# Kernel tuning notes

Hardware: AMD Instinct MI355X
Metric: run time of the kernel (lower is better)

The kernel has to match this reference:

```python
import jax, jax.numpy as jnp
import numpy as np

B, T, H = 4, 2048, 1024
NH, NKV, HD = 16, 4, 64  # heads, kv heads, head_dim

def setup_inputs() -> dict:
    key = jax.random.key(0)
    ks = jax.random.split(key, 5)
    s = 0.02
    return {
        "x": jax.random.normal(ks[0], (B, T, H), dtype=jnp.float32),
        "wq": jax.random.normal(ks[1], (H, NH * HD), dtype=jnp.float32) * s,
        "wk": jax.random.normal(ks[2], (H, NKV * HD), dtype=jnp.float32) * s,
        "wv": jax.random.normal(ks[3], (H, NKV * HD), dtype=jnp.float32) * s,
        "wo": jax.random.normal(ks[4], (NH * HD, H), dtype=jnp.float32) * s,
    }

def reference(x, wq, wk, wv, wo):
    b, t, _ = x.shape
    q = (x @ wq).reshape(b, t, NH, HD).transpose(0, 2, 1, 3)    # [B,NH,T,HD]
    k = (x @ wk).reshape(b, t, NKV, HD).transpose(0, 2, 1, 3)   # [B,NKV,T,HD]
    v = (x @ wv).reshape(b, t, NKV, HD).transpose(0, 2, 1, 3)
    n_rep = NH // NKV
    # repeat_kv: expand each kv head n_rep times along the head axis
    k_rep = jnp.repeat(k, n_rep, axis=1)                        # [B,NH,T,HD]
    v_rep = jnp.repeat(v, n_rep, axis=1)
    scale = 1.0 / np.sqrt(HD).astype(np.float32)
    scores = jnp.einsum('bhqd,bhkd->bhqk', q, k_rep) * scale    # [B,NH,T,T]
    key_pos = jnp.arange(t)[None, :]
    q_pos = jnp.arange(t)[:, None]  # past_len = 0 (no kv cache)
    causal = key_pos > q_pos                                    # [T,T]
    scores = jnp.where(causal[None, None], -jnp.inf, scores)
    probs = jax.nn.softmax(scores, axis=-1)                     # dropout is identity (eval / rate 0)
    attn = jnp.einsum('bhqk,bhkd->bhqd', probs, v_rep)          # [B,NH,T,HD]
    attn = attn.transpose(0, 2, 1, 3).reshape(b, t, NH * HD)
    return attn @ wo
```

## Files before the change

### kernel.cpp

```cpp
#include <hip/hip_runtime.h>
#include <hip/hip_bf16.h>

using bf16 = __hip_bfloat16;
typedef __attribute__((ext_vector_type(8))) short bf16x8;
typedef __attribute__((ext_vector_type(4))) short bf16x4;
typedef __attribute__((ext_vector_type(4))) float f32x4;

typedef const __attribute__((address_space(1))) void* as1_t;
typedef __attribute__((address_space(3))) void* as3_t;
__device__ __forceinline__ void load_lds16(const void* g, void* l) {
    __builtin_amdgcn_global_load_lds((as1_t)g, (as3_t)l, 16, 0, 0);
}

__global__ __launch_bounds__(256) void cast_f32_bf16(const float* __restrict__ src,
                                                     bf16* __restrict__ dst, int n4) {
    int i = (blockIdx.x * 256 + threadIdx.x);
    if (i >= n4) return;
    const float4 v = *(const float4*)(src + (long)i * 4);
    bf16 t[4];
    t[0] = __float2bfloat16(v.x);
    t[1] = __float2bfloat16(v.y);
    t[2] = __float2bfloat16(v.z);
    t[3] = __float2bfloat16(v.w);
    *(uint2*)(dst + (long)i * 4) = *(uint2*)t;
}

__global__ __launch_bounds__(256) void transpose_cast(const float* __restrict__ src,
                                                      int K, int N, bf16* __restrict__ dst) {
    __shared__ float tile[32][33];
    const int tx = threadIdx.x & 31;
    const int ty = threadIdx.x >> 5;
    const int n0 = blockIdx.x * 32;
    const int k0 = blockIdx.y * 32;
    for (int i = 0; i < 32; i += 8)
        tile[ty + i][tx] = src[(long)(k0 + ty + i) * N + n0 + tx];
    __syncthreads();
    for (int i = 0; i < 32; i += 8)
        dst[(long)(n0 + ty + i) * K + k0 + tx] = __float2bfloat16(tile[tx][ty + i]);
}

__global__ __launch_bounds__(256) void transpose_v(const bf16* __restrict__ qkv,
                                                   bf16* __restrict__ vt) {
    __shared__ bf16 tile[64][72];
    const int tb = blockIdx.x, kvh = blockIdx.y, b = blockIdx.z;
    const int r = threadIdx.x >> 3;
    const int c = (threadIdx.x & 7) * 8;
    const bf16* src = qkv + (long)(b * 2048 + tb * 64) * 1536 + 1280 + kvh * 64;
    *(uint4*)&tile[r][c]      = *(const uint4*)(src + (long)r * 1536 + c);
    *(uint4*)&tile[r + 32][c] = *(const uint4*)(src + (long)(r + 32) * 1536 + c);
    __syncthreads();
    bf16* dst = vt + (long)(b * 4 + kvh) * 64 * 2048 + tb * 64;
#pragma unroll
    for (int rr = 0; rr < 2; rr++) {
        const int d = r + rr * 32;
        bf16 t8[8];
#pragma unroll
        for (int e = 0; e < 8; e++) t8[e] = tile[c + e][d];
        *(uint4*)(dst + (long)d * 2048 + c) = *(uint4*)t8;
    }
}

template <bool BF16_OUT>
__global__ __launch_bounds__(256) void gemm_bt(const bf16* __restrict__ A,
                                               const bf16* __restrict__ Bt,
                                               void* __restrict__ C,
                                               int M, int N, int K) {
    __shared__ bf16 Ash[128 * 32];
    __shared__ bf16 Bsh[128 * 32];
    const int tid  = threadIdx.x;
    const int lane = tid & 63;
    const int wid  = tid >> 6;
    const int wm   = (wid >> 1) * 64;
    const int wn   = (wid & 1) * 64;
    const int quad = lane >> 4;
    const int l16  = lane & 15;
    const int bm = blockIdx.x, bn = blockIdx.y;

    const int r_l   = lane >> 2;
    const int cslot = lane & 3;
    const int cdat  = (cslot - (r_l >> 1)) & 3;

    const bf16* pa0 = A  + (long)(bm * 128 + wid * 32 + r_l) * K + cdat * 8;
    const bf16* pa1 = pa0 + (long)16 * K;
    const bf16* pb0 = Bt + (long)(bn * 128 + wid * 32 + r_l) * K + cdat * 8;
    const bf16* pb1 = pb0 + (long)16 * K;
    bf16* la0 = Ash + (wid * 32) * 32;
    bf16* la1 = Ash + (wid * 32 + 16) * 32;
    bf16* lb0 = Bsh + (wid * 32) * 32;
    bf16* lb1 = Bsh + (wid * 32 + 16) * 32;

    const int sw = ((quad + (l16 >> 1)) & 3) * 8;

    f32x4 acc[4][4] = {};

    for (int k0 = 0; k0 < K; k0 += 32) {
        __syncthreads();
        load_lds16(pa0 + k0, la0);
        load_lds16(pa1 + k0, la1);
        load_lds16(pb0 + k0, lb0);
        load_lds16(pb1 + k0, lb1);
        __syncthreads();

        bf16x8 af[4], bfr[4];
#pragma unroll
        for (int i = 0; i < 4; i++) af[i]  = *(const bf16x8*)&Ash[(wm + i * 16 + l16) * 32 + sw];
#pragma unroll
        for (int j = 0; j < 4; j++) bfr[j] = *(const bf16x8*)&Bsh[(wn + j * 16 + l16) * 32 + sw];
#pragma unroll
        for (int i = 0; i < 4; i++)
#pragma unroll
            for (int j = 0; j < 4; j++)
                acc[i][j] = __builtin_amdgcn_mfma_f32_16x16x32_bf16(af[i], bfr[j], acc[i][j], 0, 0, 0);
    }

#pragma unroll
    for (int i = 0; i < 4; i++) {
#pragma unroll
        for (int r = 0; r < 4; r++) {
            const long row = (long)(bm * 128 + wm + i * 16 + quad * 4 + r);
#pragma unroll
            for (int j = 0; j < 4; j++) {
                const int col = bn * 128 + wn + j * 16 + l16;
                const float v = acc[i][j][r];
                if (BF16_OUT) ((bf16*)C)[row * N + col] = __float2bfloat16(v);
                else          ((float*)C)[row * N + col] = v;
            }
        }
    }
}

__global__ __launch_bounds__(256) void attn_kernel(const bf16* __restrict__ qkv,
                                                   const bf16* __restrict__ vt,
                                                   bf16* __restrict__ attn) {
    __shared__ bf16 Ksh[64][72];
    __shared__ bf16 Vsh[64][72];

    const int tid  = threadIdx.x;
    const int lane = tid & 63;
    const int wid  = tid >> 6;
    const int quad = lane >> 4;
    const int l16  = lane & 15;
    const int h    = blockIdx.y;
    const int b    = blockIdx.z;
    const int kvh  = h >> 2;
    const int pb   = blockIdx.x;

    const float ls = 0.125f * 1.44269504f;

    bf16x4 ones;
    { short o1 = (short)0x3F80; short t4[4] = {o1, o1, o1, o1}; ones = *(const bf16x4*)t4; }

    const bf16* kg = qkv + (long)(b * 2048) * 1536 + 1024 + kvh * 64;
    const bf16* vg = vt + (long)(b * 4 + kvh) * 64 * 2048;
    const int r0 = tid >> 3;
    const int c0 = (tid & 7) * 8;

    const bf16* kp0 = kg + (long)r0 * 1536 + c0;
    const bf16* kp1 = kp0 + (long)32 * 1536;
    const bf16* vp0 = vg + (long)r0 * 2048 + c0;
    const bf16* vp1 = vp0 + (long)32 * 2048;

#pragma unroll 1
    for (int seg = 0; seg < 2; ++seg) {
        const int qb     = seg ? pb : (31 - pb);
        const int qblock = qb * 64;
        const int q0     = qblock + wid * 16;

        const bf16* qbase = qkv + (long)(b * 2048 + q0 + l16) * 1536 + h * 64;
        bf16x8 qf[2];
#pragma unroll
        for (int kf = 0; kf < 2; kf++) {
            const bf16* qp = qbase + kf * 32 + quad * 8;
            bf16 t8[8];
#pragma unroll
            for (int e = 0; e < 8; e++) t8[e] = __float2bfloat16(__bfloat162float(qp[e]) * ls);
            qf[kf] = *(const bf16x8*)t8;
        }

        f32x4 o[4] = {};
        f32x4 ol = {};

        uint4 kr0 = *(const uint4*)kp0;
        uint4 kr1 = *(const uint4*)kp1;
        uint4 vr0 = *(const uint4*)vp0;
        uint4 vr1 = *(const uint4*)vp1;

        const int nIter = qb + 1;
        for (int it = 0; it < nIter; ++it) {
            __syncthreads();
            *(uint4*)&Ksh[r0][c0]      = kr0;
            *(uint4*)&Ksh[r0 + 32][c0] = kr1;
            *(uint4*)&Vsh[r0][c0]      = vr0;
            *(uint4*)&Vsh[r0 + 32][c0] = vr1;
            __syncthreads();

            if (it + 1 < nIter) {
                const long ko = (long)(it + 1) * 64 * 1536;
                const long vo = (it + 1) * 64;
                kr0 = *(const uint4*)(kp0 + ko);
                kr1 = *(const uint4*)(kp1 + ko);
                vr0 = *(const uint4*)(vp0 + vo);
                vr1 = *(const uint4*)(vp1 + vo);
            }

            f32x4 s[4] = {};
#pragma unroll
            for (int kvt = 0; kvt < 4; kvt++)
#pragma unroll
                for (int kf = 0; kf < 2; kf++) {
                    const bf16x8 kfr = *(const bf16x8*)&Ksh[kvt * 16 + l16][kf * 32 + quad * 8];
                    s[kvt] = __builtin_amdgcn_mfma_f32_16x16x32_bf16(kfr, qf[kf], s[kvt], 0, 0, 0);
                }

            if (it == nIter - 1) {
                const int qq = wid * 16 + l16;
#pragma unroll
                for (int kvt = 0; kvt < 4; kvt++)
#pragma unroll
                    for (int r = 0; r < 4; r++)
                        if (kvt * 16 + quad * 4 + r > qq) s[kvt][r] = -1e30f;
            }

#pragma unroll
            for (int kvt = 0; kvt < 4; kvt++) {
                float2 p01, p23;
                p01.x = exp2f(s[kvt][0]);
                p01.y = exp2f(s[kvt][1]);
                p23.x = exp2f(s[kvt][2]);
                p23.y = exp2f(s[kvt][3]);
                __hip_bfloat162 pk01 = __float22bfloat162_rn(p01);
                __hip_bfloat162 pk23 = __float22bfloat162_rn(p23);
                bf16x4 pk;
                *(__hip_bfloat162*)&pk       = pk01;
                *((__hip_bfloat162*)&pk + 1) = pk23;

                ol = __builtin_amdgcn_mfma_f32_16x16x16bf16_1k(ones, pk, ol, 0, 0, 0);
#pragma unroll
                for (int dt = 0; dt < 4; dt++) {
                    const bf16x4 vf = *(const bf16x4*)&Vsh[dt * 16 + l16][kvt * 16 + quad * 4];
                    o[dt] = __builtin_amdgcn_mfma_f32_16x16x16bf16_1k(vf, pk, o[dt], 0, 0, 0);
                }
            }
        }

        const float inv = 1.f / ol[0];
        bf16* obase = attn + (long)(b * 2048 + q0 + l16) * 1024 + h * 64;
#pragma unroll
        for (int dt = 0; dt < 4; dt++) {
            bf16 t4[4];
#pragma unroll
            for (int r = 0; r < 4; r++) t4[r] = __float2bfloat16(o[dt][r] * inv);
            *(uint2*)(obase + dt * 16 + quad * 4) = *(uint2*)t4;
        }
    }
}

extern "C" void kernel_launch(void* const* d_in, const int* in_sizes, int n_in,
                              void* d_out, int out_size, void* d_ws, size_t ws_size,
                              hipStream_t stream) {
    const float* x  = (const float*)d_in[0];
    const float* wq = (const float*)d_in[1];
    const float* wk = (const float*)d_in[2];
    const float* wv = (const float*)d_in[3];
    const float* wo = (const float*)d_in[4];
    float* out = (float*)d_out;

    char* ws = (char*)d_ws;
    bf16* xb     = (bf16*)(ws);
    bf16* wqkvT  = (bf16*)(ws + 16777216);
    bf16* woT    = (bf16*)(ws + 19922944);
    bf16* qkv    = (bf16*)(ws + 22020096);
    bf16* vt     = (bf16*)(ws + 47185920);
    bf16* attn   = (bf16*)(ws + 51380224);

    cast_f32_bf16<<<8192, 256, 0, stream>>>(x, xb, 2097152);

    transpose_cast<<<dim3(32, 32), 256, 0, stream>>>(wq, 1024, 1024, wqkvT);
    transpose_cast<<<dim3(8, 32),  256, 0, stream>>>(wk, 1024, 256,  wqkvT + 1024 * 1024);
    transpose_cast<<<dim3(8, 32),  256, 0, stream>>>(wv, 1024, 256,  wqkvT + 1280 * 1024);
    transpose_cast<<<dim3(32, 32), 256, 0, stream>>>(wo, 1024, 1024, woT);

    gemm_bt<true><<<dim3(64, 12), 256, 0, stream>>>(xb, wqkvT, qkv, 8192, 1536, 1024);

    transpose_v<<<dim3(32, 4, 4), 256, 0, stream>>>(qkv, vt);

    attn_kernel<<<dim3(16, 16, 4), 256, 0, stream>>>(qkv, vt, attn);

    gemm_bt<false><<<dim3(64, 8), 256, 0, stream>>>(attn, woT, out, 8192, 1024, 1024);
}
```

Baseline: 242.5 us.

## Use 128-key tiles with XOR-swizzled LDS and MFMA priority hints in attention

Doubles the K/V tile per barrier pair from 64 to 128 keys, processing each staged tile in two 64-key halves, which halves the number of __syncthreads and global-to-LDS rounds per query block. Replaces padded LDS arrays with dense XOR-swizzled layouts to avoid bank conflicts, adds s_setprio around MFMA sequences, and sets launch_bounds occupancy hint 4. Costs more registers for the prefetch buffers and doubles LDS use, and the causal diagonal handling is now split by query-block parity.

```diff
diff --git a/kernel.cpp b/kernel.cpp
--- a/kernel.cpp
+++ b/kernel.cpp
@@ -129,11 +129,11 @@
     }
 }
 
-__global__ __launch_bounds__(256) void attn_kernel(const bf16* __restrict__ qkv,
-                                                   const bf16* __restrict__ vt,
-                                                   bf16* __restrict__ attn) {
-    __shared__ bf16 Ksh[64][72];
-    __shared__ bf16 Vsh[64][72];
+__global__ __launch_bounds__(256, 4) void attn_kernel(const bf16* __restrict__ qkv,
+                                                      const bf16* __restrict__ vt,
+                                                      bf16* __restrict__ attn) {
+    __shared__ bf16 Ksh[128 * 64];
+    __shared__ bf16 Vsh[64 * 128];
 
     const int tid  = threadIdx.x;
     const int lane = tid & 63;
@@ -152,13 +152,25 @@
 
     const bf16* kg = qkv + (long)(b * 2048) * 1536 + 1024 + kvh * 64;
     const bf16* vg = vt + (long)(b * 4 + kvh) * 64 * 2048;
-    const int r0 = tid >> 3;
-    const int c0 = (tid & 7) * 8;
-
-    const bf16* kp0 = kg + (long)r0 * 1536 + c0;
-    const bf16* kp1 = kp0 + (long)32 * 1536;
-    const bf16* vp0 = vg + (long)r0 * 2048 + c0;
-    const bf16* vp1 = vp0 + (long)32 * 2048;
+
+    const int rK = tid >> 3;
+    const int cK = (tid & 7) * 8;
+    const int rV = tid >> 4;
+    const int cV = (tid & 15) * 8;
+    const bf16* kp = kg + (long)rK * 1536 + cK;
+    const bf16* vp = vg + (long)rV * 2048 + cV;
+
+    int kwo[4], vwo[4];
+#pragma unroll
+    for (int m = 0; m < 4; m++) {
+        kwo[m] = (rK + 32 * m) * 64  + (((tid & 7)  ^ (rK & 7)) * 8);
+        vwo[m] = (rV + 16 * m) * 128 + (((tid & 15) ^ rV) * 8);
+    }
+    const int krow0   = l16 * 64;
+    const int kchunkA = ((quad)     ^ (l16 & 7)) * 8;
+    const int kchunkB = ((4 + quad) ^ (l16 & 7)) * 8;
+    const int vrow0   = l16 * 128 + (quad & 1) * 4;
+    const int vch0    = l16 ^ (quad >> 1);
 
 #pragma unroll 1
     for (int seg = 0; seg < 2; ++seg) {
@@ -180,65 +192,82 @@
         f32x4 o[4] = {};
         f32x4 ol = {};
 
-        uint4 kr0 = *(const uint4*)kp0;
-        uint4 kr1 = *(const uint4*)kp1;
-        uint4 vr0 = *(const uint4*)vp0;
-        uint4 vr1 = *(const uint4*)vp1;
-
-        const int nIter = qb + 1;
+        uint4 kr[4], vr[4];
+#pragma unroll
+        for (int m = 0; m < 4; m++) {
+            kr[m] = *(const uint4*)(kp + (long)(32 * m) * 1536);
+            vr[m] = *(const uint4*)(vp + 16 * m * 2048);
+        }
+
+        const int nIter = qb / 2 + 1;
         for (int it = 0; it < nIter; ++it) {
             __syncthreads();
-            *(uint4*)&Ksh[r0][c0]      = kr0;
-            *(uint4*)&Ksh[r0 + 32][c0] = kr1;
-            *(uint4*)&Vsh[r0][c0]      = vr0;
-            *(uint4*)&Vsh[r0 + 32][c0] = vr1;
+#pragma unroll
+            for (int m = 0; m < 4; m++) {
+                *(uint4*)&Ksh[kwo[m]] = kr[m];
+                *(uint4*)&Vsh[vwo[m]] = vr[m];
+            }
             __syncthreads();
 
             if (it + 1 < nIter) {
-                const long ko = (long)(it + 1) * 64 * 1536;
-                const long vo = (it + 1) * 64;
-                kr0 = *(const uint4*)(kp0 + ko);
-                kr1 = *(const uint4*)(kp1 + ko);
-                vr0 = *(const uint4*)(vp0 + vo);
-                vr1 = *(const uint4*)(vp1 + vo);
+                const long ko = (long)(it + 1) * 128 * 1536;
+                const int  vo = (it + 1) * 128;
+#pragma unroll
+                for (int m = 0; m < 4; m++) {
+                    kr[m] = *(const uint4*)(kp + ko + (long)(32 * m) * 1536);
+                    vr[m] = *(const uint4*)(vp + vo + 16 * m * 2048);
+                }
             }
 
-            f32x4 s[4] = {};
-#pragma unroll
-            for (int kvt = 0; kvt < 4; kvt++)
-#pragma unroll
-                for (int kf = 0; kf < 2; kf++) {
-                    const bf16x8 kfr = *(const bf16x8*)&Ksh[kvt * 16 + l16][kf * 32 + quad * 8];
-                    s[kvt] = __builtin_amdgcn_mfma_f32_16x16x32_bf16(kfr, qf[kf], s[kvt], 0, 0, 0);
+            const bool lastT = (it == nIter - 1);
+            const int nhalf = (lastT && !(qb & 1)) ? 1 : 2;
+            for (int hf = 0; hf < nhalf; ++hf) {
+                const bool diag = lastT && (hf == nhalf - 1);
+
+                f32x4 s[4] = {};
+                __builtin_amdgcn_s_setprio(1);
+#pragma unroll
+                for (int kvt = 0; kvt < 4; kvt++) {
+                    const int rbase = (hf * 64 + kvt * 16) * 64 + krow0;
+                    const bf16x8 k0 = *(const bf16x8*)&Ksh[rbase + kchunkA];
+                    s[kvt] = __builtin_amdgcn_mfma_f32_16x16x32_bf16(k0, qf[0], s[kvt], 0, 0, 0);
+                    const bf16x8 k1 = *(const bf16x8*)&Ksh[rbase + kchunkB];
+                    s[kvt] = __builtin_amdgcn_mfma_f32_16x16x32_bf16(k1, qf[1], s[kvt], 0, 0, 0);
                 }
-
-            if (it == nIter - 1) {
-                const int qq = wid * 16 + l16;
-#pragma unroll
-                for (int kvt = 0; kvt < 4; kvt++)
-#pragma unroll
-                    for (int r = 0; r < 4; r++)
-                        if (kvt * 16 + quad * 4 + r > qq) s[kvt][r] = -1e30f;
-            }
-
-#pragma unroll
-            for (int kvt = 0; kvt < 4; kvt++) {
-                float2 p01, p23;
-                p01.x = exp2f(s[kvt][0]);
-                p01.y = exp2f(s[kvt][1]);
-                p23.x = exp2f(s[kvt][2]);
-                p23.y = exp2f(s[kvt][3]);
-                __hip_bfloat162 pk01 = __float22bfloat162_rn(p01);
-                __hip_bfloat162 pk23 = __float22bfloat162_rn(p23);
-                bf16x4 pk;
-                *(__hip_bfloat162*)&pk       = pk01;
-                *((__hip_bfloat162*)&pk + 1) = pk23;
-
-                ol = __builtin_amdgcn_mfma_f32_16x16x16bf16_1k(ones, pk, ol, 0, 0, 0);
-#pragma unroll
-                for (int dt = 0; dt < 4; dt++) {
-                    const bf16x4 vf = *(const bf16x4*)&Vsh[dt * 16 + l16][kvt * 16 + quad * 4];
-                    o[dt] = __builtin_amdgcn_mfma_f32_16x16x16bf16_1k(vf, pk, o[dt], 0, 0, 0);
+                __builtin_amdgcn_s_setprio(0);
+
+                if (diag) {
+                    const int qq = wid * 16 + l16;
+#pragma unroll
+                    for (int kvt = 0; kvt < 4; kvt++)
+#pragma unroll
+                        for (int r = 0; r < 4; r++)
+                            if (kvt * 16 + quad * 4 + r > qq) s[kvt][r] = -1e30f;
+                }
+
+#pragma unroll
+                for (int kvt = 0; kvt < 4; kvt++) {
+                    float2 p01, p23;
+                    p01.x = exp2f(s[kvt][0]);
+                    p01.y = exp2f(s[kvt][1]);
+                    p23.x = exp2f(s[kvt][2]);
+                    p23.y = exp2f(s[kvt][3]);
+                    __hip_bfloat162 pk01 = __float22bfloat162_rn(p01);
+                    __hip_bfloat162 pk23 = __float22bfloat162_rn(p23);
+                    bf16x4 pk;
+                    *(__hip_bfloat162*)&pk       = pk01;
+                    *((__hip_bfloat162*)&pk + 1) = pk23;
+
+                    __builtin_amdgcn_s_setprio(1);
+                    ol = __builtin_amdgcn_mfma_f32_16x16x16bf16_1k(ones, pk, ol, 0, 0, 0);
+#pragma unroll
+                    for (int dt = 0; dt < 4; dt++) {
+                        const int vaddr = (dt * 16) * 128 + vrow0 +
+                                          ((vch0 ^ (hf * 8 + kvt * 2)) * 8);
+                        const bf16x4 vf = *(const bf16x4*)&Vsh[vaddr];
+                        o[dt] = __builtin_amdgcn_mfma_f32_16x16x16bf16_1k(vf, pk, o[dt], 0, 0, 0);
+                    }
+                    __builtin_amdgcn_s_setprio(0);
                 }
             }
         }
```

Result: slower. 359.5 us (+48.2%).
